# Optimization experiments

Hardware: AMD Instinct MI355X
Metric: run time of the kernel (lower is better)

## Reference

```python
import jax, jax.numpy as jnp
import numpy as np

B, N, IN, OUT = 16, 1000, 128, 128


def setup_inputs() -> dict:
    key = jax.random.key(0)
    ks = jax.random.split(key, 8)
    stdv = 1.0 / np.sqrt(IN + OUT)  # matches reset_param uniform(-stdv, stdv)
    def w(k):
        return jax.random.uniform(k, (N, IN + OUT, OUT), jnp.float32, -stdv, stdv)
    return {
        "xt": jax.random.normal(ks[0], (B, N, IN), jnp.float32),
        "hidden": jax.random.normal(ks[1], (1, N, OUT), jnp.float32),
        "ct_1": jax.random.normal(ks[2], (1, N, OUT), jnp.float32),
        "W_i": w(ks[3]), "b_i": jnp.zeros((N, OUT), jnp.float32),
        "W_o": w(ks[4]), "b_o": jnp.zeros((N, OUT), jnp.float32),
        "W_f": w(ks[5]), "b_f": jnp.zeros((N, OUT), jnp.float32),
        "W_c": w(ks[6]), "b_c": jnp.zeros((N, OUT), jnp.float32),
    }


def reference(xt, hidden, ct_1, W_i, b_i, W_o, b_o, W_f, b_f, W_c, b_c):
    b = xt.shape[0]
    h = jnp.broadcast_to(hidden, (b,) + hidden.shape[1:])       # [B,N,OUT]
    xh = jnp.concatenate([xt, h], axis=-1)                      # [B,N,IN+OUT]

    def gate(W, bias, act):
        # per-stock batched matmul: [B,N,K] x [N,K,O] -> [B,N,O]
        return act(jnp.einsum('bnk,nko->bno', xh, W) + bias)

    it = gate(W_i, b_i, jax.nn.sigmoid)
    ot = gate(W_o, b_o, jax.nn.sigmoid)
    ft = gate(W_f, b_f, jax.nn.sigmoid)
    chat = gate(W_c, b_c, jnp.tanh)

    ct = ft * jnp.broadcast_to(ct_1, it.shape) + it * chat
    ht = ot * jnp.tanh(ct)
    return ht, ct
```

## Files before the change

kernel.cpp:

```cpp
#include <hip/hip_runtime.h>
#include <hip/hip_bf16.h>

namespace {
constexpr int B   = 16;
constexpr int NS  = 1000;
constexpr int IN  = 128;
constexpr int OUT = 128;
constexpr int K   = 256;

typedef __attribute__((ext_vector_type(8))) short short8;
typedef __attribute__((ext_vector_type(4))) float f32x4;

__device__ __forceinline__ float fsigmoid(float x) {
  return 1.0f / (1.0f + __expf(-x));
}
__device__ __forceinline__ float ftanh(float x) {
  return 2.0f / (1.0f + __expf(-2.0f * x)) - 1.0f;
}
__device__ __forceinline__ unsigned int f2bf(float f) {
  unsigned int u = __builtin_bit_cast(unsigned int, f);
  u += 0x7fffu + ((u >> 16) & 1u);
  return u >> 16;
}
__device__ __forceinline__ unsigned int pack2(float lo, float hi) {
  return f2bf(lo) | (f2bf(hi) << 16);
}

__global__ __launch_bounds__(512, 4) void lstm_kernel(
    const float* __restrict__ xt, const float* __restrict__ hidden,
    const float* __restrict__ ct_1,
    const float* __restrict__ Wi, const float* __restrict__ bi,
    const float* __restrict__ Wo, const float* __restrict__ bo,
    const float* __restrict__ Wf, const float* __restrict__ bfp,
    const float* __restrict__ Wc, const float* __restrict__ bc,
    float* __restrict__ out) {
  __shared__ __align__(16) unsigned char smem[65536];

  const int n   = blockIdx.x;
  const int tid = threadIdx.x;
  const int wid  = tid >> 6;
  const int g    = wid >> 1;
  const int half = wid & 1;
  const int l    = tid & 63;
  const int g2   = l >> 4;
  const int c16  = l & 15;

  const float* Wg = (g == 0) ? Wi : (g == 1) ? Wo : (g == 2) ? Wf : Wc;
  const float* bg = (g == 0) ? bi : (g == 1) ? bo : (g == 2) ? bfp : bc;

  unsigned char* wbuf = smem + (wid << 13);
  const float* wcb = Wg + (size_t)n * (K * OUT) + half * 64;

  auto stage_chunk = [&](int r) {
    #pragma unroll
    for (int i = 0; i < 8; ++i) {
      const int cq = (c16 + ((i >> 1) << 2)) & 15;
      const float* src =
          wcb + (size_t)((r << 5) + (i << 2) + g2) * OUT + (cq << 2);
      __builtin_amdgcn_global_load_lds(
          (const __attribute__((address_space(1))) void*)src,
          (__attribute__((address_space(3))) void*)(wbuf + (i << 10)),
          16, 0, 0);
    }
  };
  auto load_a = [&](int r, float4& x0, float4& x1) {
    const int k = (r << 5) + (g2 << 3);
    const float* s = (k < IN) ? (xt + ((size_t)c16 * NS + n) * IN + k)
                              : (hidden + (size_t)n * OUT + (k - IN));
    x0 = *reinterpret_cast<const float4*>(s);
    x1 = *reinterpret_cast<const float4*>(s + 4);
  };

  f32x4 acc[4] = {f32x4{0,0,0,0}, f32x4{0,0,0,0}, f32x4{0,0,0,0}, f32x4{0,0,0,0}};

  stage_chunk(0);
  float4 a0, a1;
  load_a(0, a0, a1);

  #pragma unroll 1
  for (int r = 0; r < 8; ++r) {
    asm volatile("s_waitcnt vmcnt(0)" ::: "memory");

    float wv[4][8];
    #pragma unroll
    for (int t = 0; t < 4; ++t) {
      const int pb = (((((t << 2) + (c16 >> 2)) - (g2 << 2)) & 15) << 4) +
                     ((c16 & 3) << 2);
      #pragma unroll
      for (int j = 0; j < 8; ++j)
        wv[t][j] = *reinterpret_cast<const float*>(
            wbuf + (g2 << 11) + (j << 8) + pb);
    }
    uint4 au;
    au.x = pack2(a0.x, a0.y); au.y = pack2(a0.z, a0.w);
    au.z = pack2(a1.x, a1.y); au.w = pack2(a1.z, a1.w);
    const short8 af = __builtin_bit_cast(short8, au);

    asm volatile("s_waitcnt lgkmcnt(0)" ::: "memory");
    float4 na0 = a0, na1 = a1;
    if (r < 7) {
      stage_chunk(r + 1);
      load_a(r + 1, na0, na1);
    }

    #pragma unroll
    for (int t = 0; t < 4; ++t) {
      uint4 bu;
      bu.x = pack2(wv[t][0], wv[t][1]);
      bu.y = pack2(wv[t][2], wv[t][3]);
      bu.z = pack2(wv[t][4], wv[t][5]);
      bu.w = pack2(wv[t][6], wv[t][7]);
      acc[t] = __builtin_amdgcn_mfma_f32_16x16x32_bf16(
          af, __builtin_bit_cast(short8, bu), acc[t], 0, 0, 0);
    }
    a0 = na0; a1 = na1;
  }

  __syncthreads();
  float* gb = reinterpret_cast<float*>(smem);
  #pragma unroll
  for (int t = 0; t < 4; ++t) {
    const int colg = (half << 6) + (t << 4) + c16;
    const float bias = bg[(size_t)n * OUT + colg];
    #pragma unroll
    for (int r2 = 0; r2 < 4; ++r2) {
      const int b = (g2 << 2) + r2;
      gb[g * 2064 + b * 129 + colg] = acc[t][r2] + bias;
    }
  }
  __syncthreads();

  const size_t nbase = (size_t)n * OUT;
  #pragma unroll
  for (int r = 0; r < 4; ++r) {
    const int p = tid + (r << 9);
    const int b = p >> 7;
    const int o = p & 127;
    const float gi = gb[0 * 2064 + b * 129 + o];
    const float go = gb[1 * 2064 + b * 129 + o];
    const float gf = gb[2 * 2064 + b * 129 + o];
    const float gc = gb[3 * 2064 + b * 129 + o];
    const float it = fsigmoid(gi);
    const float ot = fsigmoid(go);
    const float ft = fsigmoid(gf);
    const float ch = ftanh(gc);
    const float cp = ct_1[nbase + o];
    const float ct = ft * cp + it * ch;
    const float ht = ot * ftanh(ct);
    const size_t oidx = (size_t)b * ((size_t)NS * OUT) + nbase + o;
    out[oidx] = ht;
    out[(size_t)B * NS * OUT + oidx] = ct;
  }
}
}

extern "C" void kernel_launch(void* const* d_in, const int* in_sizes, int n_in,
                              void* d_out, int out_size, void* d_ws, size_t ws_size,
                              hipStream_t stream) {
  const float* xt     = (const float*)d_in[0];
  const float* hidden = (const float*)d_in[1];
  const float* ct_1   = (const float*)d_in[2];
  const float* Wi     = (const float*)d_in[3];
  const float* bi     = (const float*)d_in[4];
  const float* Wo     = (const float*)d_in[5];
  const float* bo     = (const float*)d_in[6];
  const float* Wf     = (const float*)d_in[7];
  const float* bf     = (const float*)d_in[8];
  const float* Wc     = (const float*)d_in[9];
  const float* bc     = (const float*)d_in[10];

  lstm_kernel<<<NS, 512, 0, stream>>>(xt, hidden, ct_1, Wi, bi, Wo, bo,
                                      Wf, bf, Wc, bc,
                                      (float*)d_out);
}
```

Baseline: 108.0 us.

## Split each stock across two blocks and double-buffer weight staging

```diff
diff --git a/kernel.cpp b/kernel.cpp
--- a/kernel.cpp
+++ b/kernel.cpp
@@ -26,7 +26,7 @@
   return f2bf(lo) | (f2bf(hi) << 16);
 }
 
-__global__ __launch_bounds__(512, 4) void lstm_kernel(
+__global__ __launch_bounds__(256, 2) void lstm_kernel(
     const float* __restrict__ xt, const float* __restrict__ hidden,
     const float* __restrict__ ct_1,
     const float* __restrict__ Wi, const float* __restrict__ bi,
@@ -36,11 +36,11 @@
     float* __restrict__ out) {
   __shared__ __align__(16) unsigned char smem[65536];
 
-  const int n   = blockIdx.x;
-  const int tid = threadIdx.x;
-  const int wid  = tid >> 6;
-  const int g    = wid >> 1;
-  const int half = wid & 1;
+  const int bid  = blockIdx.x;
+  const int n    = bid >> 1;
+  const int half = bid & 1;
+  const int tid  = threadIdx.x;
+  const int g    = tid >> 6;
   const int l    = tid & 63;
   const int g2   = l >> 4;
   const int c16  = l & 15;
@@ -48,10 +48,11 @@
   const float* Wg = (g == 0) ? Wi : (g == 1) ? Wo : (g == 2) ? Wf : Wc;
   const float* bg = (g == 0) ? bi : (g == 1) ? bo : (g == 2) ? bfp : bc;
 
-  unsigned char* wbuf = smem + (wid << 13);
+  unsigned char* buf0 = smem + (g << 14);
+  unsigned char* buf1 = buf0 + 8192;
   const float* wcb = Wg + (size_t)n * (K * OUT) + half * 64;
 
-  auto stage_chunk = [&](int r) {
+  auto stage_chunk = [&](int r, unsigned char* buf) {
     #pragma unroll
     for (int i = 0; i < 8; ++i) {
       const int cq = (c16 + ((i >> 1) << 2)) & 15;
@@ -59,7 +60,7 @@
           wcb + (size_t)((r << 5) + (i << 2) + g2) * OUT + (cq << 2);
       __builtin_amdgcn_global_load_lds(
           (const __attribute__((address_space(1))) void*)src,
-          (__attribute__((address_space(3))) void*)(wbuf + (i << 10)),
+          (__attribute__((address_space(3))) void*)(buf + (i << 10)),
           16, 0, 0);
     }
   };
@@ -73,13 +74,9 @@
 
   f32x4 acc[4] = {f32x4{0,0,0,0}, f32x4{0,0,0,0}, f32x4{0,0,0,0}, f32x4{0,0,0,0}};
 
-  stage_chunk(0);
-  float4 a0, a1;
-  load_a(0, a0, a1);
-
-  #pragma unroll 1
-  for (int r = 0; r < 8; ++r) {
-    asm volatile("s_waitcnt vmcnt(0)" ::: "memory");
+  auto kstep = [&](int r, float4& cA0, float4& cA1, unsigned char* buf) {
+    if (r >= 7) asm volatile("s_waitcnt vmcnt(0)" ::: "memory");
+    else        asm volatile("s_waitcnt vmcnt(10)" ::: "memory");
 
     float wv[4][8];
     #pragma unroll
@@ -89,18 +86,18 @@
       #pragma unroll
       for (int j = 0; j < 8; ++j)
         wv[t][j] = *reinterpret_cast<const float*>(
-            wbuf + (g2 << 11) + (j << 8) + pb);
+            buf + (g2 << 11) + (j << 8) + pb);
     }
+    asm volatile("s_waitcnt lgkmcnt(0)" ::: "memory");
+
     uint4 au;
-    au.x = pack2(a0.x, a0.y); au.y = pack2(a0.z, a0.w);
-    au.z = pack2(a1.x, a1.y); au.w = pack2(a1.z, a1.w);
+    au.x = pack2(cA0.x, cA0.y); au.y = pack2(cA0.z, cA0.w);
+    au.z = pack2(cA1.x, cA1.y); au.w = pack2(cA1.z, cA1.w);
     const short8 af = __builtin_bit_cast(short8, au);
 
-    asm volatile("s_waitcnt lgkmcnt(0)" ::: "memory");
-    float4 na0 = a0, na1 = a1;
-    if (r < 7) {
-      stage_chunk(r + 1);
-      load_a(r + 1, na0, na1);
+    if (r < 6) {
+      load_a(r + 2, cA0, cA1);
+      stage_chunk(r + 2, buf);
     }
 
     #pragma unroll
@@ -113,19 +110,30 @@
       acc[t] = __builtin_amdgcn_mfma_f32_16x16x32_bf16(
           af, __builtin_bit_cast(short8, bu), acc[t], 0, 0, 0);
     }
-    a0 = na0; a1 = na1;
+  };
+
+  float4 aA0, aA1, aB0, aB1;
+  load_a(0, aA0, aA1);
+  stage_chunk(0, buf0);
+  load_a(1, aB0, aB1);
+  stage_chunk(1, buf1);
+
+  #pragma unroll 1
+  for (int rr = 0; rr < 8; rr += 2) {
+    kstep(rr,     aA0, aA1, buf0);
+    kstep(rr + 1, aB0, aB1, buf1);
   }
 
   __syncthreads();
   float* gb = reinterpret_cast<float*>(smem);
   #pragma unroll
   for (int t = 0; t < 4; ++t) {
-    const int colg = (half << 6) + (t << 4) + c16;
-    const float bias = bg[(size_t)n * OUT + colg];
+    const int coll = (t << 4) + c16;
+    const float bias = bg[(size_t)n * OUT + half * 64 + coll];
     #pragma unroll
     for (int r2 = 0; r2 < 4; ++r2) {
       const int b = (g2 << 2) + r2;
-      gb[g * 2064 + b * 129 + colg] = acc[t][r2] + bias;
+      gb[g * 1040 + b * 65 + coll] = acc[t][r2] + bias;
     }
   }
   __syncthreads();
@@ -133,13 +141,14 @@
   const size_t nbase = (size_t)n * OUT;
   #pragma unroll
   for (int r = 0; r < 4; ++r) {
-    const int p = tid + (r << 9);
-    const int b = p >> 7;
-    const int o = p & 127;
-    const float gi = gb[0 * 2064 + b * 129 + o];
-    const float go = gb[1 * 2064 + b * 129 + o];
-    const float gf = gb[2 * 2064 + b * 129 + o];
-    const float gc = gb[3 * 2064 + b * 129 + o];
+    const int p    = tid + (r << 8);
+    const int b    = p >> 6;
+    const int coll = p & 63;
+    const int o    = half * 64 + coll;
+    const float gi = gb[0 * 1040 + b * 65 + coll];
+    const float go = gb[1 * 1040 + b * 65 + coll];
+    const float gf = gb[2 * 1040 + b * 65 + coll];
+    const float gc = gb[3 * 1040 + b * 65 + coll];
     const float it = fsigmoid(gi);
     const float ot = fsigmoid(go);
     const float ft = fsigmoid(gf);
@@ -169,7 +178,7 @@
   const float* Wc     = (const float*)d_in[9];
   const float* bc     = (const float*)d_in[10];
 
-  lstm_kernel<<<NS, 512, 0, stream>>>(xt, hidden, ct_1, Wi, bi, Wo, bo,
-                                      Wf, bf, Wc, bc,
-                                      (float*)d_out);
+  lstm_kernel<<<2 * NS, 256, 0, stream>>>(xt, hidden, ct_1, Wi, bi, Wo, bo,
+                                          Wf, bf, Wc, bc,
+                                          (float*)d_out);
 }
```

Result: no change. 109.6 us (+1.5%).
